# Kernel tuning notes

Hardware: AMD Instinct MI355X
Metric: run time of the kernel (lower is better)

Reference implementation:

```python
import jax, jax.numpy as jnp
import numpy as np
import math

B, L, D_IN, H, N, N_CLASSES = 16, 8192, 128, 256, 64, 10
DT_MIN, DT_MAX = 1e-3, 1e-1


def setup_inputs() -> dict:
    key = jax.random.key(0)
    ks = jax.random.split(key, 16)
    x = jax.random.normal(ks[0], (B, L, D_IN), dtype=jnp.float32)
    # fc1
    W1 = jax.random.normal(ks[1], (D_IN, H), dtype=jnp.float32) / np.sqrt(D_IN)
    b1 = jnp.zeros((H,), jnp.float32)
    # LayerNorm
    ln_g = jnp.ones((H,), jnp.float32)
    ln_b = jnp.zeros((H,), jnp.float32)
    # S4D kernel params (standard S4D-Lin init)
    log_dt = jax.random.uniform(ks[2], (H,), jnp.float32) * (
        math.log(DT_MAX) - math.log(DT_MIN)) + math.log(DT_MIN)
    log_A_real = jnp.log(0.5 * jnp.ones((H, N // 2), jnp.float32))
    A_imag = math.pi * jnp.broadcast_to(jnp.arange(N // 2, dtype=jnp.float32), (H, N // 2))
    C_re = jax.random.normal(ks[3], (H, N // 2), dtype=jnp.float32)
    C_im = jax.random.normal(ks[4], (H, N // 2), dtype=jnp.float32)
    Dp = jax.random.normal(ks[5], (H,), dtype=jnp.float32)
    # output_linear: Conv1d(H, 2H, 1) + GLU
    Wo = jax.random.normal(ks[6], (H, 2 * H), dtype=jnp.float32) / np.sqrt(H)
    bo = jnp.zeros((2 * H,), jnp.float32)
    # head
    W2 = jax.random.normal(ks[7], (H, 512), dtype=jnp.float32) / np.sqrt(H)
    b2 = jnp.zeros((512,), jnp.float32)
    W3 = jax.random.normal(ks[8], (512, N_CLASSES), dtype=jnp.float32) / np.sqrt(512)
    b3 = jnp.zeros((N_CLASSES,), jnp.float32)
    return dict(x=x, W1=W1, b1=b1, ln_g=ln_g, ln_b=ln_b, log_dt=log_dt,
                log_A_real=log_A_real, A_imag=A_imag, C_re=C_re, C_im=C_im,
                Dp=Dp, Wo=Wo, bo=bo, W2=W2, b2=b2, W3=W3, b3=b3)


def _s4d_kernel(log_dt, log_A_real, A_imag, C_re, C_im, length):
    dt = jnp.exp(log_dt)[:, None]                       # (H,1)
    A = -jnp.exp(log_A_real) + 1j * A_imag               # (H,N/2) complex
    dtA = A * dt                                          # (H,N/2)
    C = (C_re + 1j * C_im) * (jnp.exp(dtA) - 1.0) / A     # (H,N/2)
    l = jnp.arange(length, dtype=jnp.float32)
    vand = jnp.exp(dtA[:, :, None] * l)                   # (H,N/2,L) Vandermonde
    return 2.0 * jnp.einsum('hn,hnl->hl', C, vand).real   # (H,L)


def reference(x, W1, b1, ln_g, ln_b, log_dt, log_A_real, A_imag, C_re, C_im,
              Dp, Wo, bo, W2, b2, W3, b3):
    # fc1 + ReLU
    h = jax.nn.relu(x @ W1 + b1)                          # (B,L,H)
    # LayerNorm
    mu = jnp.mean(h, axis=-1, keepdims=True)
    var = jnp.mean(jnp.square(h - mu), axis=-1, keepdims=True)
    u = (h - mu) * jax.lax.rsqrt(var + 1e-5) * ln_g + ln_b
    # S4D: FFT long convolution along L
    Lseq = u.shape[1]
    k = _s4d_kernel(log_dt, log_A_real, A_imag, C_re, C_im, Lseq)  # (H,L)
    n_fft = 2 * Lseq
    k_f = jnp.fft.rfft(k, n=n_fft, axis=-1)               # (H,F)
    u_f = jnp.fft.rfft(u, n=n_fft, axis=1)                # (B,F,H)
    y = jnp.fft.irfft(u_f * k_f.T[None], n=n_fft, axis=1)[:, :Lseq]  # (B,L,H)
    y = y + u * Dp                                        # skip D term
    y = jax.nn.gelu(y, approximate=False)
    # output_linear: pointwise conv to 2H + GLU
    v = y @ Wo + bo                                       # (B,L,2H)
    y = v[..., :H] * jax.nn.sigmoid(v[..., H:])           # GLU
    # max-pool over sequence
    pooled = jnp.max(y, axis=1)                           # (B,H)
    f = jax.nn.leaky_relu(pooled @ W2 + b2, negative_slope=0.01)
    logits = f @ W3 + b3                                  # (B,n_classes)
    Y_hat = jnp.argmax(logits, axis=0)                    # matches torch dim=0
    return logits, Y_hat
```

## Files before the change

### kernel.cpp

```cpp
#include <hip/hip_runtime.h>
#include <math.h>

typedef float f32x4 __attribute__((ext_vector_type(4)));
typedef short bf16x8 __attribute__((ext_vector_type(8)));

#define BB 16
#define LL 8192
#define DIN 128
#define HH 256
#define NCH 32
#define TCH 256

#define U_OFF    0ull
#define PRM_OFF  67108864ull
#define KK_OFF   67371008ull
#define WKE_OFF  67633152ull
#define F_OFF    109576192ull
#define SB_OFF   117964800ull
#define SBH_OFF  134742016ull
#define W1T_OFF  151519232ull
#define WOT_OFF  151584768ull
#define PART_OFF 151846912ull
#define POOL_OFF 152895488ull
#define FC_OFF   152911872ull

static __device__ __forceinline__ unsigned short f2b(float f){
  unsigned int u = __float_as_uint(f);
  return (unsigned short)((u + 0x7fffu + ((u>>16)&1u)) >> 16);
}
static __device__ __forceinline__ float b2f(unsigned int h){
  return __uint_as_float((h & 0xffffu)<<16);
}

static __device__ __forceinline__ float gelu_t(float v){
  float vv = v*v;
  float p  = fmaf(0.044715f, vv, 1.0f);
  float z  = v*p*(-1.5957691216057308f);
  float e  = __expf(z);
  return v*__builtin_amdgcn_rcpf(1.0f + e);
}

typedef __attribute__((address_space(3))) unsigned int lds_u32_t;
typedef const __attribute__((address_space(1))) unsigned int glb_u32_t;
static __device__ __forceinline__ void gl16(const void* g, void* l){
  __builtin_amdgcn_global_load_lds((glb_u32_t*)g, (lds_u32_t*)l, 16, 0, 0);
}

__global__ __launch_bounds__(256) void kp_all(
    const float* __restrict__ log_dt, const float* __restrict__ log_A_real,
    const float* __restrict__ A_imag, const float* __restrict__ C_re,
    const float* __restrict__ C_im, float* __restrict__ prm,
    const float* __restrict__ Wo, unsigned short* __restrict__ wot,
    const float* __restrict__ W1, unsigned short* __restrict__ w1t,
    unsigned short* __restrict__ wke, unsigned short* __restrict__ fb){
  int bid = blockIdx.x;
  int t = threadIdx.x;
  if (bid < 32){
    int id = bid*256 + t;
    int h = id >> 5;
    float dt = expf(log_dt[h]);
    float Ar = -expf(log_A_real[id]);
    float Ai = A_imag[id];
    float dr = Ar*dt, di = Ai*dt;
    float ear = expf(dr);
    float are = ear*cosf(di), aim = ear*sinf(di);
    float er = are - 1.0f, ei = aim;
    float den = 1.0f/(Ar*Ar + Ai*Ai);
    float Br = (er*Ar + ei*Ai)*den;
    float Bi = (ei*Ar - er*Ai)*den;
    float c_r = C_re[id], c_i = C_im[id];
    float cre = 2.0f*(c_r*Br - c_i*Bi);
    float cim = 2.0f*(c_r*Bi + c_i*Br);
    double phi = (double)di*(double)TCH;
    float eT = expf(dr*(float)TCH);
    float aTre = eT*(float)cos(phi);
    float aTim = eT*(float)sin(phi);
    prm[id]         = are;  prm[8192  + id] = aim;
    prm[16384 + id] = cre;  prm[24576 + id] = cim;
    prm[32768 + id] = aTre; prm[40960 + id] = aTim;
    prm[49152 + id] = dr;   prm[57344 + id] = di;
  } else if (bid < 544){
    int id = (bid-32)*256 + t;
    int k = id >> 9, n = id & 511;
    wot[n*256 + k] = f2b(Wo[id]);
  } else if (bid < 672){
    int id = (bid-544)*256 + t;
    int k = id >> 8, n = id & 255;
    w1t[((k>>3)<<11) + (n<<3) + (k&7)] = f2b(W1[k*256 + n]);
  } else if (bid < 2720){
    int bid2 = bid - 672;
    int h = bid2 >> 3, ng = bid2 & 7;
    int nn = t & 3;
    int n  = (ng<<2) + nn;
    int hn = (h<<5) + n;
    float dt = expf(log_dt[h]);
    float Ar = -expf(log_A_real[hn]);
    float Ai = A_imag[hn];
    float dr = Ar*dt, di = Ai*dt;
    float ear = expf(dr);
    float are = ear*cosf(di), aim = ear*sinf(di);
    float er = are - 1.0f, ei = aim;
    float den = 1.0f/(Ar*Ar + Ai*Ai);
    float Br = (er*Ar + ei*Ai)*den;
    float Bi = (ei*Ar - er*Ai)*den;
    float c_r = C_re[hn], c_i = C_im[hn];
    float cre = 2.0f*(c_r*Br - c_i*Bi);
    float cim = 2.0f*(c_r*Bi + c_i*Br);
    int q = 32 + ng, c = nn << 1;
    unsigned short* W = wke + (size_t)h*81920 + ((size_t)q<<11) + c;
    int mb = t >> 2;
    #pragma unroll
    for (int i = 0; i < 4; ++i){
      int m = mb + (i<<6);
      float fm = (float)(m+1);
      float E  = expf(dr*fm);
      float ph = di*fm;
      float car = E*cosf(ph), sar = E*sinf(ph);
      float zr = cre*car - cim*sar;
      float zi = cre*sar + cim*car;
      *(unsigned int*)(W + (m<<3)) = ((unsigned int)f2b(-zi)<<16) | f2b(zr);
    }
  } else {
    int bid3 = bid - 2720;
    int h = bid3 >> 5, n = bid3 & 31;
    int hn = (h<<5) + n;
    float dt = expf(log_dt[h]);
    float Ar = -expf(log_A_real[hn]);
    float Ai = A_imag[hn];
    float dr = Ar*dt, di = Ai*dt;
    int j = t;
    float fp = (float)(255 - j);
    float E  = expf(dr*fp);
    float ph = di*fp;
    unsigned short* Fh = fb + ((size_t)h<<14) + (n<<9);
    Fh[j]       = f2b(E*cosf(ph));
    Fh[256 + j] = f2b(E*sinf(ph));
  }
}

__global__ __launch_bounds__(256) void kp_khw(const float* __restrict__ prm,
                                              const float* __restrict__ Dp,
                                              unsigned short* __restrict__ wke){
  __shared__ float kh[256];
  int h = blockIdx.x;
  int d = threadIdx.x;
  {
    float fd = (float)d;
    float s = 0.f;
    #pragma unroll 8
    for (int n = 0; n < 32; ++n){
      int i0 = (h<<5) + n;
      float dr = prm[49152 + i0], di = prm[57344 + i0];
      float cr = prm[16384 + i0], ci = prm[24576 + i0];
      float e = expf(dr*fd);
      float ph = di*fd;
      s += e*(cr*cosf(ph) - ci*sinf(ph));
    }
    kh[d] = s;
  }
  __syncthreads();
  int m = threadIdx.x;
  float dp = Dp[h];
  unsigned short* W = wke + (size_t)h*81920;
  for (int j4 = 0; j4 < 256; j4 += 4){
    ushort4 o;
    float v0 = (j4+0 <= m) ? kh[m-j4-0] : 0.f; if (j4+0 == m) v0 += dp;
    float v1 = (j4+1 <= m) ? kh[m-j4-1] : 0.f; if (j4+1 == m) v1 += dp;
    float v2 = (j4+2 <= m) ? kh[m-j4-2] : 0.f; if (j4+2 == m) v2 += dp;
    float v3 = (j4+3 <= m) ? kh[m-j4-3] : 0.f; if (j4+3 == m) v3 += dp;
    o.x = f2b(v0); o.y = f2b(v1); o.z = f2b(v2); o.w = f2b(v3);
    *(ushort4*)(W + (((j4>>3)<<11)) + (m<<3) + (j4&7)) = o;
  }
}

__global__ __launch_bounds__(512, 4) void k1_fc1_ln(const float* __restrict__ x,
    const unsigned short* __restrict__ w1t, const float* __restrict__ b1,
    const float* __restrict__ lng, const float* __restrict__ lnb,
    unsigned short* __restrict__ u){
  __shared__ unsigned short sX[64*128];
  __shared__ float sRed[4][64][2];
  int t = threadIdx.x;
  int lane = t & 63, wid = t >> 6;
  int wr = wid >> 2, wc = wid & 3;
  int g0 = blockIdx.x << 6;
  int b = g0 >> 13, l0 = g0 & 8191;
  {
    int r = t >> 3, kq = (t & 7) << 4;
    const float* xr = x + (size_t)(g0 + r)*DIN + kq;
    #pragma unroll
    for (int i = 0; i < 4; ++i){
      float4 v = *(const float4*)(xr + i*4);
      ushort4 o; o.x=f2b(v.x); o.y=f2b(v.y); o.z=f2b(v.z); o.w=f2b(v.w);
      int k0 = kq + i*4;
      int q = k0 >> 3;
      *(ushort4*)&sX[(r<<7) + ((q ^ (r&7))<<3) + (k0&7)] = o;
    }
  }
  __syncthreads();
  f32x4 acc[2][4];
  #pragma unroll
  for (int mi = 0; mi < 2; ++mi)
    #pragma unroll
    for (int ni = 0; ni < 4; ++ni) acc[mi][ni] = (f32x4){0.f,0.f,0.f,0.f};
  #pragma unroll
  for (int kt = 0; kt < 4; ++kt){
    bf16x8 af[2];
    #pragma unroll
    for (int mi = 0; mi < 2; ++mi){
      int m = (wr<<5) + (mi<<4) + (lane&15);
      int q = (kt<<2) + (lane>>4);
      af[mi] = *(const bf16x8*)&sX[(m<<7) + ((q ^ (m&7))<<3)];
    }
    #pragma unroll
    for (int ni = 0; ni < 4; ++ni){
      int hcol = (wc<<6) + (ni<<4) + (lane&15);
      bf16x8 bf = *(const bf16x8*)(w1t + (((kt<<2) + (lane>>4))<<11) + (hcol<<3));
      acc[0][ni] = __builtin_amdgcn_mfma_f32_16x16x32_bf16(af[0], bf, acc[0][ni], 0,0,0);
      acc[1][ni] = __builtin_amdgcn_mfma_f32_16x16x32_bf16(af[1], bf, acc[1][ni], 0,0,0);
    }
  }
  float bv[4];
  #pragma unroll
  for (int ni = 0; ni < 4; ++ni) bv[ni] = b1[(wc<<6) + (ni<<4) + (lane&15)];
  float s1[2][4] = {{0,0,0,0},{0,0,0,0}}, s2[2][4] = {{0,0,0,0},{0,0,0,0}};
  #pragma unroll
  for (int mi = 0; mi < 2; ++mi)
    #pragma unroll
    for (int ni = 0; ni < 4; ++ni)
      #pragma unroll
      for (int rr = 0; rr < 4; ++rr){
        float v = acc[mi][ni][rr] + bv[ni];
        v = v > 0.f ? v : 0.f;
        acc[mi][ni][rr] = v;
        s1[mi][rr] += v; s2[mi][rr] = fmaf(v, v, s2[mi][rr]);
      }
  #pragma unroll
  for (int off = 1; off < 16; off <<= 1)
    #pragma unroll
    for (int mi = 0; mi < 2; ++mi)
      #pragma unroll
      for (int rr = 0; rr < 4; ++rr){
        s1[mi][rr] += __shfl_xor(s1[mi][rr], off);
        s2[mi][rr] += __shfl_xor(s2[mi][rr], off);
      }
  if ((lane & 15) == 0){
    #pragma unroll
    for (int mi = 0; mi < 2; ++mi)
      #pragma unroll
      for (int rr = 0; rr < 4; ++rr){
        int row = (wr<<5) + (mi<<4) + ((lane>>4)<<2) + rr;
        sRed[wc][row][0] = s1[mi][rr];
        sRed[wc][row][1] = s2[mi][rr];
      }
  }
  __syncthreads();
  float mu[2][4], rs[2][4];
  #pragma unroll
  for (int mi = 0; mi < 2; ++mi)
    #pragma unroll
    for (int rr = 0; rr < 4; ++rr){
      int row = (wr<<5) + (mi<<4) + ((lane>>4)<<2) + rr;
      float t1 = sRed[0][row][0] + sRed[1][row][0] + sRed[2][row][0] + sRed[3][row][0];
      float t2 = sRed[0][row][1] + sRed[1][row][1] + sRed[2][row][1] + sRed[3][row][1];
      float m_ = t1*(1.f/256.f);
      mu[mi][rr] = m_;
      rs[mi][rr] = rsqrtf(t2*(1.f/256.f) - m_*m_ + 1e-5f);
    }
  #pragma unroll
  for (int ni = 0; ni < 4; ++ni){
    int hcol = (wc<<6) + (ni<<4) + (lane&15);
    float g = lng[hcol], bb = lnb[hcol];
    #pragma unroll
    for (int mi = 0; mi < 2; ++mi){
      ushort4 o;
      o.x = f2b((acc[mi][ni][0]-mu[mi][0])*rs[mi][0]*g + bb);
      o.y = f2b((acc[mi][ni][1]-mu[mi][1])*rs[mi][1]*g + bb);
      o.z = f2b((acc[mi][ni][2]-mu[mi][2])*rs[mi][2]*g + bb);
      o.w = f2b((acc[mi][ni][3]-mu[mi][3])*rs[mi][3]*g + bb);
      *(ushort4*)(u + (((size_t)(b*HH + hcol))<<13) + l0 + (wr<<5) + (mi<<4) + ((lane>>4)<<2)) = o;
    }
  }
}

__global__ __launch_bounds__(256, 4) void k2a_states(const unsigned short* __restrict__ u,
                                                     const unsigned short* __restrict__ fb,
                                                     const float* __restrict__ prm,
                                                     unsigned short* __restrict__ sbh){
  __shared__ unsigned short sA2[2][64*32];
  __shared__ unsigned short sB2[2][128*32];
  __shared__ unsigned short sS[128*64];
  int bid = blockIdx.x;
  int lb = ((bid & 7) << 7) + (bid >> 3);
  int h = lb >> 2, nt = lb & 3;
  int t = threadIdx.x;
  int lane = t & 63, wid = t >> 6;
  int wr = wid >> 1, wc = wid & 1;

  int ar0 = t >> 2;
  int asl = t & 3;
  int asw = (asl ^ ((ar0 >> 1) & 3)) << 3;
  const unsigned short* aS = fb + ((size_t)h<<14) + ar0*256 + asw;

  int lcol = t >> 2;
  int bsl  = t & 3;
  int bsw  = (bsl ^ ((lcol >> 1) & 3)) << 3;
  int bc0  = (nt << 7) + lcol;
  int bc1  = bc0 + 64;
  const unsigned short* bS0 = u + (((size_t)((bc0>>5)*HH + h)) << 13) + ((bc0&31) << 8) + bsw;
  const unsigned short* bS1 = u + (((size_t)((bc1>>5)*HH + h)) << 13) + ((bc1&31) << 8) + bsw;

  unsigned short* dA[2]  = { &sA2[0][wid<<9], &sA2[1][wid<<9] };
  unsigned short* dB0[2] = { &sB2[0][wid<<9], &sB2[1][wid<<9] };
  unsigned short* dB1[2] = { &sB2[0][2048 + (wid<<9)], &sB2[1][2048 + (wid<<9)] };

  int aoff[2], boff[4];
  #pragma unroll
  for (int mi = 0; mi < 2; ++mi){
    int m = (wr<<5) + (mi<<4) + (lane&15);
    aoff[mi] = (m<<5) + (((lane>>4) ^ ((m>>1)&3))<<3);
  }
  #pragma unroll
  for (int ni = 0; ni < 4; ++ni){
    int c = (wc<<6) + (ni<<4) + (lane&15);
    boff[ni] = (c<<5) + (((lane>>4) ^ ((c>>1)&3))<<3);
  }

  f32x4 acc[2][4];
  #pragma unroll
  for (int mi = 0; mi < 2; ++mi)
    #pragma unroll
    for (int ni = 0; ni < 4; ++ni) acc[mi][ni] = (f32x4){0.f,0.f,0.f,0.f};

  gl16(aS, dA[0]);
  gl16(bS0, dB0[0]);
  gl16(bS1, dB1[0]);
  __syncthreads();

  #pragma unroll 2
  for (int kt = 0; kt < 8; ++kt){
    int cur = kt & 1;
    if (kt < 7){
      int k1o = (kt+1) << 5;
      gl16(aS  + k1o, dA[cur^1]);
      gl16(bS0 + k1o, dB0[cur^1]);
      gl16(bS1 + k1o, dB1[cur^1]);
    }
    const unsigned short* Ab = sA2[cur];
    const unsigned short* Bb = sB2[cur];
    bf16x8 af[2], bfv[4];
    #pragma unroll
    for (int mi = 0; mi < 2; ++mi) af[mi] = *(const bf16x8*)(Ab + aoff[mi]);
    #pragma unroll
    for (int ni = 0; ni < 4; ++ni) bfv[ni] = *(const bf16x8*)(Bb + boff[ni]);
    #pragma unroll
    for (int mi = 0; mi < 2; ++mi)
      #pragma unroll
      for (int ni = 0; ni < 4; ++ni)
        acc[mi][ni] = __builtin_amdgcn_mfma_f32_16x16x32_bf16(af[mi], bfv[ni], acc[mi][ni], 0,0,0);
    __syncthreads();
  }

  #pragma unroll
  for (int ni = 0; ni < 4; ++ni){
    int lc = (wc<<6) + (ni<<4) + (lane&15);
    #pragma unroll
    for (int mi = 0; mi < 2; ++mi){
      int srow = (wr<<5) + (mi<<4) + ((lane>>4)<<2);
      ushort4 o;
      o.x = f2b(acc[mi][ni][0]); o.y = f2b(acc[mi][ni][1]);
      o.z = f2b(acc[mi][ni][2]); o.w = f2b(acc[mi][ni][3]);
      *(ushort4*)&sS[(lc<<6) + srow] = o;
    }
  }
  __syncthreads();

  if (t < 128){
    int bloc = t >> 5, n = t & 31;
    int b = (nt<<2) + bloc;
    int i0 = (h<<5) + n;
    float aTr = prm[32768 + i0], aTi = prm[40960 + i0];
    size_t base = (((size_t)b*HH + h)*NCH)*64 + (n<<1);
    float ir = 0.f, ii = 0.f;
    for (int c = 0; c < NCH; ++c){
      *(unsigned int*)(sbh + base + (size_t)(c<<6)) = ((unsigned int)f2b(ii)<<16) | f2b(ir);
      unsigned int rw = *(const unsigned int*)&sS[((bloc<<5) + c)*64 + (n<<1)];
      float lr = b2f(rw), li = b2f(rw>>16);
      float nr = fmaf(aTr, ir, fmaf(-aTi, ii, lr));
      float ni_ = fmaf(aTr, ii, fmaf(aTi, ir, li));
      ir = nr; ii = ni_;
    }
  }
}

__global__ __launch_bounds__(512, 4) void k2c_emit(unsigned short* __restrict__ uy,
                                                   const unsigned short* __restrict__ wke,
                                                   const unsigned short* __restrict__ sbh){
  __shared__ unsigned short sB[2][128*32];
  __shared__ unsigned short sW[8][1152];
  int bid = blockIdx.x;
  int lb = ((bid & 7) << 7) + (bid >> 3);
  int h = lb >> 2, nt = lb & 3;
  int t = threadIdx.x;
  int lane = t & 63, wid = t >> 6;
  int wr = wid >> 1, wc = wid & 1;

  const unsigned short* wkeh = wke + (size_t)h*81920;

  int bcol = t >> 2;
  int bsl  = t & 3;
  int bsw  = (bsl ^ ((bcol >> 1) & 3)) << 3;
  int bcg  = (nt << 7) + bcol;
  int bb   = bcg >> 5, chk = bcg & 31;
  const unsigned short* bSU = uy  + (((size_t)(bb*HH + h)) << 13) + (chk << 8) + bsw;
  const unsigned short* bSS = sbh + (((size_t)bb*HH + h)*NCH + chk)*64 + bsw;

  unsigned short* dB0 = &sB[0][wid<<9];
  unsigned short* dB0b= &sB[1][wid<<9];

  int am[4];
  #pragma unroll
  for (int mi = 0; mi < 4; ++mi) am[mi] = (wr<<6) + (mi<<4) + (lane&15);
  int boff[4];
  #pragma unroll
  for (int ni = 0; ni < 4; ++ni){
    int c = (wc<<6) + (ni<<4) + (lane&15);
    boff[ni] = (c<<5) + (((lane>>4) ^ ((c>>1)&3))<<3);
  }

  f32x4 acc[4][4];
  #pragma unroll
  for (int mi = 0; mi < 4; ++mi)
    #pragma unroll
    for (int ni = 0; ni < 4; ++ni) acc[mi][ni] = (f32x4){0.f,0.f,0.f,0.f};

  gl16(bSU, dB0);
  __syncthreads();

  #pragma unroll 2
  for (int kt = 0; kt < 10; ++kt){
    int cur = kt & 1;
    if (kt < 9){
      int k1o = (kt+1) << 5;
      const unsigned short* bs = (kt+1 < 8) ? (bSU + k1o) : (bSS + ((kt+1-8) << 5));
      gl16(bs, cur ? dB0 : dB0b);
    }
    int q = (kt<<2) + (lane>>4);
    const unsigned short* Ab = wkeh + ((size_t)q<<11);
    const unsigned short* Bb = sB[cur];
    bf16x8 af[4], bfv[4];
    #pragma unroll
    for (int mi = 0; mi < 4; ++mi) af[mi] = *(const bf16x8*)(Ab + (am[mi]<<3));
    #pragma unroll
    for (int ni = 0; ni < 4; ++ni) bfv[ni] = *(const bf16x8*)(Bb + boff[ni]);
    #pragma unroll
    for (int mi = 0; mi < 4; ++mi)
      #pragma unroll
      for (int ni = 0; ni < 4; ++ni)
        acc[mi][ni] = __builtin_amdgcn_mfma_f32_16x16x32_bf16(af[mi], bfv[ni], acc[mi][ni], 0,0,0);
    __syncthreads();
  }

  unsigned short* wbase = sW[wid];
  int col16 = lane & 15;
  int rcol  = lane >> 2;
  int rseg  = lane & 3;
  #pragma unroll
  for (int ni = 0; ni < 4; ++ni){
    #pragma unroll
    for (int mi = 0; mi < 4; ++mi){
      int mloc = (mi<<4) + ((lane>>4)<<2);
      ushort4 o;
      #pragma unroll
      for (int rr = 0; rr < 4; ++rr)
        ((unsigned short*)&o)[rr] = f2b(gelu_t(acc[mi][ni][rr]));
      *(ushort4*)&wbase[col16*72 + mloc] = o;
    }
    int bcO = (nt<<7) + (wc<<6) + (ni<<4) + rcol;
    unsigned short* op = uy + (((size_t)((bcO>>5)*HH + h))<<13) + ((bcO&31)<<8)
                       + (wr<<6) + (rseg<<4);
    uint4 va = *(const uint4*)&wbase[rcol*72 + (rseg<<4)];
    uint4 vb = *(const uint4*)&wbase[rcol*72 + (rseg<<4) + 8];
    *(uint4*)op       = va;
    *(uint4*)(op + 8) = vb;
  }
}

__global__ __launch_bounds__(512) void k3_glu(const unsigned short* __restrict__ y,
                                              const unsigned short* __restrict__ wot,
                                              const float* __restrict__ bo,
                                              float* __restrict__ part){
  __shared__ unsigned short sA[128*64];
  __shared__ unsigned short sB[2][128*64];
  __shared__ float smax[2][256];
  int t = threadIdx.x;
  int lane = t & 63, wid = t >> 6;
  int wg = wid >> 2;
  int wl = wid & 3;
  int bid = blockIdx.x;
  int lb = ((bid & 7) << 8) + (bid >> 3);
  int js2 = lb & 1, mb = (lb >> 1) & 63, b = lb >> 7;
  int js = (js2 << 1) + wg;
  f32x4 acc[2][8];
  #pragma unroll
  for (int i = 0; i < 2; ++i)
    #pragma unroll
    for (int j = 0; j < 8; ++j)
      acc[i][j] = (f32x4){0.f,0.f,0.f,0.f};

  for (int kt = 0; kt < 4; ++kt){
    __syncthreads();
    {
      int hl = t & 63, g = t >> 6;
      const unsigned short* yb = y + (((size_t)(b*HH + (kt<<6) + hl))<<13) + (mb<<7);
      int qh = hl >> 3, hm = hl & 7;
      #pragma unroll
      for (int rep = 0; rep < 2; ++rep){
        int m0 = ((rep<<3) + g) << 3;
        float4 v = *(const float4*)(yb + m0);
        const unsigned short* pv = (const unsigned short*)&v;
        #pragma unroll
        for (int j = 0; j < 8; ++j){
          int m = m0 + j;
          sA[(m<<6) + ((qh ^ (m&7))<<3) + hm] = pv[j];
        }
      }
    }
    {
      int tt = t & 255;
      #pragma unroll
      for (int p = 0; p < 4; ++p){
        int idx = (p<<8) + tt;
        int row = idx >> 3, sl = idx & 7;
        int ng = (row < 64) ? ((js<<6) + row) : (256 + (js<<6) + row - 64);
        const float4 v = *(const float4*)(wot + (ng<<8) + (kt<<6) + (sl<<3));
        *(float4*)&sB[wg][(row<<6) + ((sl ^ (row&7))<<3)] = v;
      }
    }
    __syncthreads();
    #pragma unroll
    for (int kk = 0; kk < 2; ++kk){
      bf16x8 af[2], bfr[8];
      #pragma unroll
      for (int mi = 0; mi < 2; ++mi){
        int r = (wl<<5) + (mi<<4) + (lane&15);
        int sl = (kk<<2) + (lane>>4);
        af[mi] = *(const bf16x8*)&sA[(r<<6) + ((sl ^ (r&7))<<3)];
      }
      #pragma unroll
      for (int ni = 0; ni < 8; ++ni){
        int r = (ni<<4) + (lane&15);
        int sl = (kk<<2) + (lane>>4);
        bfr[ni] = *(const bf16x8*)&sB[wg][(r<<6) + ((sl ^ (r&7))<<3)];
      }
      #pragma unroll
      for (int ni = 0; ni < 8; ++ni)
        #pragma unroll
        for (int mi = 0; mi < 2; ++mi)
          acc[mi][ni] = __builtin_amdgcn_mfma_f32_16x16x32_bf16(af[mi], bfr[ni], acc[mi][ni], 0, 0, 0);
    }
  }

  float bo1[4], bo2[4];
  #pragma unroll
  for (int ni = 0; ni < 4; ++ni){
    int col = (js<<6) + (ni<<4) + (lane&15);
    bo1[ni] = bo[col]; bo2[ni] = bo[256 + col];
  }
  #pragma unroll
  for (int ni = 0; ni < 4; ++ni){
    float m = -3.4e38f;
    #pragma unroll
    for (int mi = 0; mi < 2; ++mi)
      #pragma unroll
      for (int r = 0; r < 4; ++r){
        float v1 = acc[mi][ni][r] + bo1[ni];
        float v2 = acc[mi][ni+4][r] + bo2[ni];
        float g = v1 * (1.0f/(1.0f + __expf(-v2)));
        m = fmaxf(m, g);
      }
    m = fmaxf(m, __shfl_xor(m, 16));
    m = fmaxf(m, __shfl_xor(m, 32));
    if (lane < 16) smax[wg][(wl<<6) + (ni<<4) + lane] = m;
  }
  __syncthreads();
  if (t < 128){
    int wg2 = t >> 6, tt = t & 63;
    int jso = (js2 << 1) + wg2;
    float m = fmaxf(fmaxf(smax[wg2][tt], smax[wg2][64+tt]),
                    fmaxf(smax[wg2][128+tt], smax[wg2][192+tt]));
    part[(((size_t)b<<6) + mb)*256 + (jso<<6) + tt] = m;
  }
}

__global__ void k35_pool(const float* __restrict__ part, float* __restrict__ pool){
  int b = blockIdx.x, j = threadIdx.x;
  float m = -3.4e38f;
  for (int mb = 0; mb < 64; ++mb)
    m = fmaxf(m, part[(((size_t)b<<6) + mb)*256 + j]);
  pool[(b<<8) + j] = m;
}
__global__ void k4a_fc2(const float* __restrict__ pool, const float* __restrict__ W2,
                        const float* __restrict__ b2, float* __restrict__ f){
  int id = blockIdx.x*256 + threadIdx.x;
  int b = id >> 9, ko = id & 511;
  float s = b2[ko];
  #pragma unroll 8
  for (int hh = 0; hh < 256; ++hh)
    s = fmaf(pool[(b<<8) + hh], W2[hh*512 + ko], s);
  f[id] = s > 0.0f ? s : 0.01f*s;
}
__global__ void k4b_head(const float* __restrict__ f, const float* __restrict__ W3,
                         const float* __restrict__ b3, float* __restrict__ out){
  __shared__ float lg[160];
  int t = threadIdx.x;
  if (t < 160){
    int b = t/10, c = t - 10*b;
    float s = b3[c];
    #pragma unroll 8
    for (int ko = 0; ko < 512; ++ko)
      s = fmaf(f[(b<<9) + ko], W3[ko*10 + c], s);
    lg[t] = s;
    out[t] = s;
  }
  __syncthreads();
  if (t < 10){
    int bi = 0; float bvv = lg[t];
    for (int b2i = 1; b2i < 16; ++b2i){
      float vv = lg[b2i*10 + t];
      if (vv > bvv){ bvv = vv; bi = b2i; }
    }
    out[160 + t] = (float)bi;
  }
}

extern "C" void kernel_launch(void* const* d_in, const int* in_sizes, int n_in,
                              void* d_out, int out_size, void* d_ws, size_t ws_size,
                              hipStream_t stream) {
  const float* x      = (const float*)d_in[0];
  const float* W1     = (const float*)d_in[1];
  const float* b1     = (const float*)d_in[2];
  const float* lng    = (const float*)d_in[3];
  const float* lnb    = (const float*)d_in[4];
  const float* log_dt = (const float*)d_in[5];
  const float* logA   = (const float*)d_in[6];
  const float* Aim    = (const float*)d_in[7];
  const float* Cre    = (const float*)d_in[8];
  const float* Cim    = (const float*)d_in[9];
  const float* Dp     = (const float*)d_in[10];
  const float* Wo     = (const float*)d_in[11];
  const float* bo     = (const float*)d_in[12];
  const float* W2     = (const float*)d_in[13];
  const float* b2     = (const float*)d_in[14];
  const float* W3     = (const float*)d_in[15];
  const float* b3     = (const float*)d_in[16];
  char* wsb = (char*)d_ws;
  unsigned short* u   = (unsigned short*)(wsb + U_OFF);
  float* prm          = (float*)(wsb + PRM_OFF);
  unsigned short* wke = (unsigned short*)(wsb + WKE_OFF);
  unsigned short* fb  = (unsigned short*)(wsb + F_OFF);
  unsigned short* sbh = (unsigned short*)(wsb + SBH_OFF);
  unsigned short* w1t = (unsigned short*)(wsb + W1T_OFF);
  unsigned short* wot = (unsigned short*)(wsb + WOT_OFF);
  float* part         = (float*)(wsb + PART_OFF);
  float* pool         = (float*)(wsb + POOL_OFF);
  float* fbuf         = (float*)(wsb + FC_OFF);
  float* out          = (float*)d_out;

  kp_all   <<<dim3(10912),dim3(256), 0, stream>>>(log_dt, logA, Aim, Cre, Cim, prm,
                                                  Wo, wot, W1, w1t, wke, fb);
  kp_khw   <<<dim3(256),  dim3(256), 0, stream>>>(prm, Dp, wke);
  k1_fc1_ln<<<dim3(2048), dim3(512), 0, stream>>>(x, w1t, b1, lng, lnb, u);
  k2a_states<<<dim3(1024),dim3(256), 0, stream>>>(u, fb, prm, sbh);
  k2c_emit <<<dim3(1024), dim3(512), 0, stream>>>(u, wke, sbh);
  k3_glu   <<<dim3(2048), dim3(512), 0, stream>>>(u, wot, bo, part);
  k35_pool <<<dim3(16),   dim3(256), 0, stream>>>(part, pool);
  k4a_fc2  <<<dim3(32),   dim3(256), 0, stream>>>(pool, W2, b2, fbuf);
  k4b_head <<<dim3(1),    dim3(256), 0, stream>>>(fbuf, W3, b3, out);
}
```

Measured before the change: 243.4 us.

## Fuse chunk-state computation and scan into the emit kernel

Removes the separate k2a_states kernel. k2c_emit now computes the per-chunk state projections with an extra MFMA stream during its main loop, using the F matrix re-laid out in fragment-friendly order by kp_all. It then runs the sequential chunk scan in shared memory and feeds the resulting states into the last two k-tiles. This drops one launch and the global round-trip through sbh, and avoids re-reading u. In exchange it adds a serial scan section inside the emit kernel and changes launch bounds, which may affect occupancy.

```diff
diff --git a/kernel.cpp b/kernel.cpp
--- a/kernel.cpp
+++ b/kernel.cpp
@@ -122,19 +122,22 @@
     }
   } else {
     int bid3 = bid - 2720;
-    int h = bid3 >> 5, n = bid3 & 31;
+    int h = bid3 >> 5, q = bid3 & 31;
+    int row = t >> 2, kc = (t & 3) << 1;
+    int n = row >> 1;
     int hn = (h<<5) + n;
     float dt = expf(log_dt[h]);
     float Ar = -expf(log_A_real[hn]);
     float Ai = A_imag[hn];
     float dr = Ar*dt, di = Ai*dt;
-    int j = t;
-    float fp = (float)(255 - j);
-    float E  = expf(dr*fp);
-    float ph = di*fp;
-    unsigned short* Fh = fb + ((size_t)h<<14) + (n<<9);
-    Fh[j]       = f2b(E*cosf(ph));
-    Fh[256 + j] = f2b(E*sinf(ph));
+    float p0 = (float)(255 - ((q<<3) + kc));
+    float p1 = p0 - 1.0f;
+    float E0 = expf(dr*p0), E1 = expf(dr*p1);
+    float v0, v1;
+    if (row & 1){ v0 = E0*sinf(di*p0); v1 = E1*sinf(di*p1); }
+    else        { v0 = E0*cosf(di*p0); v1 = E1*cosf(di*p1); }
+    unsigned short* W = fb + ((size_t)h<<14) + (q<<9) + (row<<3) + kc;
+    *(unsigned int*)W = ((unsigned int)f2b(v1)<<16) | f2b(v0);
   }
 }
 
@@ -282,119 +285,10 @@
   }
 }
 
-__global__ __launch_bounds__(256, 4) void k2a_states(const unsigned short* __restrict__ u,
-                                                     const unsigned short* __restrict__ fb,
-                                                     const float* __restrict__ prm,
-                                                     unsigned short* __restrict__ sbh){
-  __shared__ unsigned short sA2[2][64*32];
-  __shared__ unsigned short sB2[2][128*32];
-  __shared__ unsigned short sS[128*64];
-  int bid = blockIdx.x;
-  int lb = ((bid & 7) << 7) + (bid >> 3);
-  int h = lb >> 2, nt = lb & 3;
-  int t = threadIdx.x;
-  int lane = t & 63, wid = t >> 6;
-  int wr = wid >> 1, wc = wid & 1;
-
-  int ar0 = t >> 2;
-  int asl = t & 3;
-  int asw = (asl ^ ((ar0 >> 1) & 3)) << 3;
-  const unsigned short* aS = fb + ((size_t)h<<14) + ar0*256 + asw;
-
-  int lcol = t >> 2;
-  int bsl  = t & 3;
-  int bsw  = (bsl ^ ((lcol >> 1) & 3)) << 3;
-  int bc0  = (nt << 7) + lcol;
-  int bc1  = bc0 + 64;
-  const unsigned short* bS0 = u + (((size_t)((bc0>>5)*HH + h)) << 13) + ((bc0&31) << 8) + bsw;
-  const unsigned short* bS1 = u + (((size_t)((bc1>>5)*HH + h)) << 13) + ((bc1&31) << 8) + bsw;
-
-  unsigned short* dA[2]  = { &sA2[0][wid<<9], &sA2[1][wid<<9] };
-  unsigned short* dB0[2] = { &sB2[0][wid<<9], &sB2[1][wid<<9] };
-  unsigned short* dB1[2] = { &sB2[0][2048 + (wid<<9)], &sB2[1][2048 + (wid<<9)] };
-
-  int aoff[2], boff[4];
-  #pragma unroll
-  for (int mi = 0; mi < 2; ++mi){
-    int m = (wr<<5) + (mi<<4) + (lane&15);
-    aoff[mi] = (m<<5) + (((lane>>4) ^ ((m>>1)&3))<<3);
-  }
-  #pragma unroll
-  for (int ni = 0; ni < 4; ++ni){
-    int c = (wc<<6) + (ni<<4) + (lane&15);
-    boff[ni] = (c<<5) + (((lane>>4) ^ ((c>>1)&3))<<3);
-  }
-
-  f32x4 acc[2][4];
-  #pragma unroll
-  for (int mi = 0; mi < 2; ++mi)
-    #pragma unroll
-    for (int ni = 0; ni < 4; ++ni) acc[mi][ni] = (f32x4){0.f,0.f,0.f,0.f};
-
-  gl16(aS, dA[0]);
-  gl16(bS0, dB0[0]);
-  gl16(bS1, dB1[0]);
-  __syncthreads();
-
-  #pragma unroll 2
-  for (int kt = 0; kt < 8; ++kt){
-    int cur = kt & 1;
-    if (kt < 7){
-      int k1o = (kt+1) << 5;
-      gl16(aS  + k1o, dA[cur^1]);
-      gl16(bS0 + k1o, dB0[cur^1]);
-      gl16(bS1 + k1o, dB1[cur^1]);
-    }
-    const unsigned short* Ab = sA2[cur];
-    const unsigned short* Bb = sB2[cur];
-    bf16x8 af[2], bfv[4];
-    #pragma unroll
-    for (int mi = 0; mi < 2; ++mi) af[mi] = *(const bf16x8*)(Ab + aoff[mi]);
-    #pragma unroll
-    for (int ni = 0; ni < 4; ++ni) bfv[ni] = *(const bf16x8*)(Bb + boff[ni]);
-    #pragma unroll
-    for (int mi = 0; mi < 2; ++mi)
-      #pragma unroll
-      for (int ni = 0; ni < 4; ++ni)
-        acc[mi][ni] = __builtin_amdgcn_mfma_f32_16x16x32_bf16(af[mi], bfv[ni], acc[mi][ni], 0,0,0);
-    __syncthreads();
-  }
-
-  #pragma unroll
-  for (int ni = 0; ni < 4; ++ni){
-    int lc = (wc<<6) + (ni<<4) + (lane&15);
-    #pragma unroll
-    for (int mi = 0; mi < 2; ++mi){
-      int srow = (wr<<5) + (mi<<4) + ((lane>>4)<<2);
-      ushort4 o;
-      o.x = f2b(acc[mi][ni][0]); o.y = f2b(acc[mi][ni][1]);
-      o.z = f2b(acc[mi][ni][2]); o.w = f2b(acc[mi][ni][3]);
-      *(ushort4*)&sS[(lc<<6) + srow] = o;
-    }
-  }
-  __syncthreads();
-
-  if (t < 128){
-    int bloc = t >> 5, n = t & 31;
-    int b = (nt<<2) + bloc;
-    int i0 = (h<<5) + n;
-    float aTr = prm[32768 + i0], aTi = prm[40960 + i0];
-    size_t base = (((size_t)b*HH + h)*NCH)*64 + (n<<1);
-    float ir = 0.f, ii = 0.f;
-    for (int c = 0; c < NCH; ++c){
-      *(unsigned int*)(sbh + base + (size_t)(c<<6)) = ((unsigned int)f2b(ii)<<16) | f2b(ir);
-      unsigned int rw = *(const unsigned int*)&sS[((bloc<<5) + c)*64 + (n<<1)];
-      float lr = b2f(rw), li = b2f(rw>>16);
-      float nr = fmaf(aTr, ir, fmaf(-aTi, ii, lr));
-      float ni_ = fmaf(aTr, ii, fmaf(aTi, ir, li));
-      ir = nr; ii = ni_;
-    }
-  }
-}
-
-__global__ __launch_bounds__(512, 4) void k2c_emit(unsigned short* __restrict__ uy,
-                                                   const unsigned short* __restrict__ wke,
-                                                   const unsigned short* __restrict__ sbh){
+__global__ __launch_bounds__(512) void k2c_emit(unsigned short* __restrict__ uy,
+                                                const unsigned short* __restrict__ wke,
+                                                const unsigned short* __restrict__ fF,
+                                                const float* __restrict__ prm){
   __shared__ unsigned short sB[2][128*32];
   __shared__ unsigned short sW[8][1152];
   int bid = blockIdx.x;
@@ -405,14 +299,14 @@
   int wr = wid >> 1, wc = wid & 1;
 
   const unsigned short* wkeh = wke + (size_t)h*81920;
+  const unsigned short* fFh  = fF + ((size_t)h<<14);
 
   int bcol = t >> 2;
   int bsl  = t & 3;
   int bsw  = (bsl ^ ((bcol >> 1) & 3)) << 3;
   int bcg  = (nt << 7) + bcol;
   int bb   = bcg >> 5, chk = bcg & 31;
-  const unsigned short* bSU = uy  + (((size_t)(bb*HH + h)) << 13) + (chk << 8) + bsw;
-  const unsigned short* bSS = sbh + (((size_t)bb*HH + h)*NCH + chk)*64 + bsw;
+  const unsigned short* bSU = uy + (((size_t)(bb*HH + h)) << 13) + (chk << 8) + bsw;
 
   unsigned short* dB0 = &sB[0][wid<<9];
   unsigned short* dB0b= &sB[1][wid<<9];
@@ -420,6 +314,7 @@
   int am[4];
   #pragma unroll
   for (int mi = 0; mi < 4; ++mi) am[mi] = (wr<<6) + (mi<<4) + (lane&15);
+  int am1 = (wr<<4) + (lane&15);
   int boff[4];
   #pragma unroll
   for (int ni = 0; ni < 4; ++ni){
@@ -432,17 +327,18 @@
   for (int mi = 0; mi < 4; ++mi)
     #pragma unroll
     for (int ni = 0; ni < 4; ++ni) acc[mi][ni] = (f32x4){0.f,0.f,0.f,0.f};
+  f32x4 acc1[4];
+  #pragma unroll
+  for (int ni = 0; ni < 4; ++ni) acc1[ni] = (f32x4){0.f,0.f,0.f,0.f};
 
   gl16(bSU, dB0);
   __syncthreads();
 
   #pragma unroll 2
-  for (int kt = 0; kt < 10; ++kt){
+  for (int kt = 0; kt < 8; ++kt){
     int cur = kt & 1;
-    if (kt < 9){
-      int k1o = (kt+1) << 5;
-      const unsigned short* bs = (kt+1 < 8) ? (bSU + k1o) : (bSS + ((kt+1-8) << 5));
-      gl16(bs, cur ? dB0 : dB0b);
+    if (kt < 7){
+      gl16(bSU + ((kt+1) << 5), cur ? dB0 : dB0b);
     }
     int q = (kt<<2) + (lane>>4);
     const unsigned short* Ab = wkeh + ((size_t)q<<11);
@@ -450,6 +346,7 @@
     bf16x8 af[4], bfv[4];
     #pragma unroll
     for (int mi = 0; mi < 4; ++mi) af[mi] = *(const bf16x8*)(Ab + (am[mi]<<3));
+    bf16x8 af1 = *(const bf16x8*)(fFh + (q<<9) + (am1<<3));
     #pragma unroll
     for (int ni = 0; ni < 4; ++ni) bfv[ni] = *(const bf16x8*)(Bb + boff[ni]);
     #pragma unroll
@@ -457,7 +354,58 @@
       #pragma unroll
       for (int ni = 0; ni < 4; ++ni)
         acc[mi][ni] = __builtin_amdgcn_mfma_f32_16x16x32_bf16(af[mi], bfv[ni], acc[mi][ni], 0,0,0);
+    #pragma unroll
+    for (int ni = 0; ni < 4; ++ni)
+      acc1[ni] = __builtin_amdgcn_mfma_f32_16x16x32_bf16(af1, bfv[ni], acc1[ni], 0,0,0);
     __syncthreads();
+  }
+
+  #pragma unroll
+  for (int ni = 0; ni < 4; ++ni){
+    int col = (wc<<6) + (ni<<4) + (lane&15);
+    int sw = (col>>1)&3;
+    #pragma unroll
+    for (int rr = 0; rr < 4; ++rr){
+      int krow = (wr<<4) + ((lane>>4)<<2) + rr;
+      sB[krow>>5][(col<<5) + ((((krow&31)>>3) ^ sw)<<3) + (krow&7)] = f2b(acc1[ni][rr]);
+    }
+  }
+  __syncthreads();
+  if (t < 128){
+    int bloc = t >> 5, n = t & 31;
+    int i0 = (h<<5) + n;
+    float aTr = prm[32768 + i0], aTi = prm[40960 + i0];
+    int k0 = n << 1;
+    int tile = k0 >> 5, kk = k0 & 31;
+    int slot = kk >> 3, k7 = kk & 7;
+    float ir = 0.f, ii = 0.f;
+    for (int c = 0; c < 32; ++c){
+      int col = (bloc<<5) + c;
+      int addr = (col<<5) + ((slot ^ ((col>>1)&3))<<3) + k7;
+      unsigned int rw = *(unsigned int*)&sB[tile][addr];
+      *(unsigned int*)&sB[tile][addr] = ((unsigned int)f2b(ii)<<16) | f2b(ir);
+      float lr = b2f(rw), li = b2f(rw>>16);
+      float nr = fmaf(aTr, ir, fmaf(-aTi, ii, lr));
+      float ni_ = fmaf(aTr, ii, fmaf(aTi, ir, li));
+      ir = nr; ii = ni_;
+    }
+  }
+  __syncthreads();
+  #pragma unroll
+  for (int kt = 8; kt < 10; ++kt){
+    int q = (kt<<2) + (lane>>4);
+    const unsigned short* Ab = wkeh + ((size_t)q<<11);
+    const unsigned short* Bb = sB[kt-8];
+    bf16x8 af[4], bfv[4];
+    #pragma unroll
+    for (int mi = 0; mi < 4; ++mi) af[mi] = *(const bf16x8*)(Ab + (am[mi]<<3));
+    #pragma unroll
+    for (int ni = 0; ni < 4; ++ni) bfv[ni] = *(const bf16x8*)(Bb + boff[ni]);
+    #pragma unroll
+    for (int mi = 0; mi < 4; ++mi)
+      #pragma unroll
+      for (int ni = 0; ni < 4; ++ni)
+        acc[mi][ni] = __builtin_amdgcn_mfma_f32_16x16x32_bf16(af[mi], bfv[ni], acc[mi][ni], 0,0,0);
   }
 
   unsigned short* wbase = sW[wid];
@@ -658,7 +606,6 @@
   float* prm          = (float*)(wsb + PRM_OFF);
   unsigned short* wke = (unsigned short*)(wsb + WKE_OFF);
   unsigned short* fb  = (unsigned short*)(wsb + F_OFF);
-  unsigned short* sbh = (unsigned short*)(wsb + SBH_OFF);
   unsigned short* w1t = (unsigned short*)(wsb + W1T_OFF);
   unsigned short* wot = (unsigned short*)(wsb + WOT_OFF);
   float* part         = (float*)(wsb + PART_OFF);
@@ -670,8 +617,7 @@
                                                   Wo, wot, W1, w1t, wke, fb);
   kp_khw   <<<dim3(256),  dim3(256), 0, stream>>>(prm, Dp, wke);
   k1_fc1_ln<<<dim3(2048), dim3(512), 0, stream>>>(x, w1t, b1, lng, lnb, u);
-  k2a_states<<<dim3(1024),dim3(256), 0, stream>>>(u, fb, prm, sbh);
-  k2c_emit <<<dim3(1024), dim3(512), 0, stream>>>(u, wke, sbh);
+  k2c_emit <<<dim3(1024), dim3(512), 0, stream>>>(u, wke, fb, prm);
   k3_glu   <<<dim3(2048), dim3(512), 0, stream>>>(u, wot, bo, part);
   k35_pool <<<dim3(16),   dim3(256), 0, stream>>>(part, pool);
   k4a_fc2  <<<dim3(32),   dim3(256), 0, stream>>>(pool, W2, b2, fbuf);
```

Result: no change. 246.6 us (+1.3%).
